# Kernel optimization log

Measured on AMD Instinct MI355X. Metric: run time of the kernel, lower is better.

The kernel has to match this reference:

```python
import jax, jax.numpy as jnp
import numpy as np

B, N, DIN, DOUT, K = 4, 2048, 512, 512, 3


def setup_inputs() -> dict:
    key = jax.random.key(0)
    ks = jax.random.split(key, 8)
    X = jax.random.normal(ks[0], (B, N, DIN), dtype=jnp.float32)
    A = jax.random.uniform(ks[1], (B, N, N), dtype=jnp.float32)
    # Linear_V: dimIn -> dimOut
    Wv = jax.random.normal(ks[2], (DIN, DOUT), dtype=jnp.float32) * 0.02
    bv = jax.random.normal(ks[3], (DOUT,), dtype=jnp.float32) * 0.02
    # alpha: Linear(2*dimOut -> 1) followed by LeakyReLU(0.2)
    aw = jax.random.normal(ks[4], (2 * DOUT, 1), dtype=jnp.float32) * 0.05
    ab = jax.random.normal(ks[5], (1,), dtype=jnp.float32) * 0.05
    # K parallel linears dimIn -> dimOut
    Wk = jax.random.normal(ks[6], (K, DIN, DOUT), dtype=jnp.float32) * 0.02
    bk = jax.random.normal(ks[7], (K, DOUT), dtype=jnp.float32) * 0.02
    return {"X": X, "A": A, "Wv": Wv, "bv": bv, "aw": aw, "ab": ab, "Wk": Wk, "bk": bk}


def reference(X, A, Wv, bv, aw, ab, Wk, bk):
    d = Wv.shape[1]
    Xw = X @ Wv + bv                      # (B, N, dOut)
    # att_input[b,i,j] = concat(Xw[b,j], Xw[b,i]); alpha is affine, so
    # alpha(att_input)[b,i,j] = aw1.Xw[b,j] + aw2.Xw[b,i] + ab  (GAT-style split)
    sj = Xw @ aw[:d, 0]                   # (B, N) contribution of column index j
    si = Xw @ aw[d:, 0]                   # (B, N) contribution of row index i
    e = jax.nn.leaky_relu(sj[:, None, :] + si[:, :, None] + ab[0], negative_slope=0.2)
    alpha_matrix = A * jnp.exp(e)         # (B, N, N)
    transition = alpha_matrix / (jnp.sum(alpha_matrix, axis=-1, keepdims=True) + 1e-12)
    H = jnp.zeros(X.shape[:-1] + (d,), dtype=X.dtype)
    Xk = X
    for k in range(Wk.shape[0]):          # K is a small static constant
        H = H + Xk @ Wk[k] + bk[k]
        Xk = jnp.einsum('bij,bjd->bid', transition, Xk)
    return jax.nn.relu(H)
```

## Files before the change

kernel.cpp:

```cpp
#include <hip/hip_runtime.h>

typedef float f32x4 __attribute__((ext_vector_type(4)));
typedef short s16x8 __attribute__((ext_vector_type(8)));
typedef unsigned short u16;
typedef unsigned char u8;
typedef u16 u16x4v __attribute__((ext_vector_type(4)));
typedef u16 u16x8v __attribute__((ext_vector_type(8)));

#define NB 4
#define NN 2048
#define DI 512
#define DOUTC 512
#define KP 3
#define KCAT 1536

__device__ __forceinline__ u16 f2b(float f) {
  unsigned u = __builtin_bit_cast(unsigned, f);
  unsigned r = u + 0x7fffu + ((u >> 16) & 1u);
  return (u16)(r >> 16);
}
__device__ __forceinline__ float b2f(u16 h) {
  unsigned u = (unsigned)h << 16;
  return __builtin_bit_cast(float, u);
}
__device__ __forceinline__ unsigned pk4_fp8(float a, float b, float c, float d) {
  int r = __builtin_amdgcn_cvt_pk_fp8_f32(a, b, 0, false);
  r = __builtin_amdgcn_cvt_pk_fp8_f32(c, d, r, true);
  return (unsigned)r;
}

__global__ void prep_all(const float* __restrict__ Wv, const float* __restrict__ aw,
                         const float* __restrict__ bk, const float* __restrict__ bv,
                         const float* __restrict__ ab,
                         float* u, float* v, float* bsum, float* cc) {
  if (blockIdx.x < 2) {
    int c = blockIdx.x * 256 + threadIdx.x;
    float a1 = 0.f, a2 = 0.f;
    const float* row = Wv + (size_t)c * DOUTC;
    for (int d = 0; d < DOUTC; ++d) {
      float w = row[d];
      a1 += w * aw[d];
      a2 += w * aw[DOUTC + d];
    }
    u[c] = a1; v[c] = a2;
    bsum[c] = bk[c] + bk[DOUTC + c] + bk[2 * DOUTC + c];
  } else if (threadIdx.x < 64) {
    int l = threadIdx.x;
    float s = 0.f;
    for (int d = l; d < DOUTC; d += 64) s += bv[d] * (aw[d] + aw[DOUTC + d]);
    for (int o = 32; o; o >>= 1) s += __shfl_down(s, o);
    if (l == 0) cc[0] = s + ab[0];
  }
}

__global__ void transWk_k(const float* __restrict__ in, u16* __restrict__ out) {
  __shared__ u16 tile[64][65];
  const float* inS = in + (size_t)blockIdx.z * DI * DOUTC;
  int r0 = blockIdx.y * 64, c0 = blockIdx.x * 64;
  int t = threadIdx.x;
#pragma unroll
  for (int p = 0; p < 4; ++p) {
    int g = t + p * 256;
    int r = g >> 4, c4 = (g & 15) << 2;
    f32x4 x = *(const f32x4*)(inS + (size_t)(r0 + r) * DOUTC + c0 + c4);
    tile[r][c4+0] = f2b(x[0]); tile[r][c4+1] = f2b(x[1]);
    tile[r][c4+2] = f2b(x[2]); tile[r][c4+3] = f2b(x[3]);
  }
  __syncthreads();
#pragma unroll
  for (int p = 0; p < 4; ++p) {
    int g = t + p * 256;
    int oc = g >> 4, o4 = (g & 15) << 2;
    u16x4v wv;
    wv[0] = tile[o4+0][oc]; wv[1] = tile[o4+1][oc];
    wv[2] = tile[o4+2][oc]; wv[3] = tile[o4+3][oc];
    *(u16x4v*)(out + (size_t)(c0 + oc) * KCAT + blockIdx.z * 512 + r0 + o4) = wv;
  }
}

__global__ void transX_k(const float* __restrict__ X, u8* __restrict__ XbT,
                         u16* __restrict__ X123,
                         const float* __restrict__ u, const float* __restrict__ v,
                         float* __restrict__ Pj, float* __restrict__ Pi) {
  __shared__ u16 tile[64][65];
  int z = blockIdx.z;
  const float* inS = X + (size_t)z * NN * DI;
  int r0 = blockIdx.y * 64, c0 = blockIdx.x * 64;
  int t = threadIdx.x, cl = t & 15;
  f32x4 u4 = *(const f32x4*)(u + c0 + cl * 4);
  f32x4 v4 = *(const f32x4*)(v + c0 + cl * 4);
#pragma unroll
  for (int p = 0; p < 4; ++p) {
    int g = t + p * 256;
    int r = g >> 4, c4 = cl << 2;
    f32x4 x = *(const f32x4*)(inS + (size_t)(r0 + r) * DI + c0 + c4);
    u16x4v bv4;
    bv4[0] = f2b(x[0]); bv4[1] = f2b(x[1]); bv4[2] = f2b(x[2]); bv4[3] = f2b(x[3]);
    tile[r][c4+0] = bv4[0]; tile[r][c4+1] = bv4[1];
    tile[r][c4+2] = bv4[2]; tile[r][c4+3] = bv4[3];
    *(u16x4v*)(X123 + (size_t)z * NN * KCAT + (size_t)(r0 + r) * KCAT + c0 + c4) = bv4;
    float s1 = x[0]*u4[0] + x[1]*u4[1] + x[2]*u4[2] + x[3]*u4[3];
    float s2 = x[0]*v4[0] + x[1]*v4[1] + x[2]*v4[2] + x[3]*v4[3];
#pragma unroll
    for (int m = 1; m < 16; m <<= 1) {
      s1 += __shfl_xor(s1, m);
      s2 += __shfl_xor(s2, m);
    }
    if (cl == 0) {
      int gr = z * NN + r0 + r;
      Pj[(size_t)blockIdx.x * (NB * NN) + gr] = s1;
      Pi[(size_t)blockIdx.x * (NB * NN) + gr] = s2;
    }
  }
  __syncthreads();
#pragma unroll
  for (int p = 0; p < 4; ++p) {
    int g = t + p * 256;
    int oc = g >> 4, o4 = (g & 15) << 2;
    unsigned w4 = pk4_fp8(b2f(tile[o4+0][oc]), b2f(tile[o4+1][oc]),
                          b2f(tile[o4+2][oc]), b2f(tile[o4+3][oc]));
    *(unsigned*)(XbT + (size_t)z * DI * NN + (size_t)(c0 + oc) * NN + r0 + o4) = w4;
  }
}

__global__ void sjsi_red(const float* __restrict__ Pj, const float* __restrict__ Pi,
                         float* __restrict__ sj, float* __restrict__ si) {
  int r = blockIdx.x * 256 + threadIdx.x;
  float s1 = 0.f, s2 = 0.f;
#pragma unroll
  for (int cb = 0; cb < 8; ++cb) {
    s1 += Pj[(size_t)cb * (NB * NN) + r];
    s2 += Pi[(size_t)cb * (NB * NN) + r];
  }
  sj[r] = s1; si[r] = s2;
}

__global__ void tmat_kernel(const float* __restrict__ Aa, const float* __restrict__ sj,
                            const float* __restrict__ si, const float* __restrict__ ccp,
                            u8* __restrict__ T, int rowbase) {
  int wid = threadIdx.x >> 6, lane = threadIdx.x & 63;
  int lr = blockIdx.x * 4 + wid;
  int gi = rowbase + lr;
  int b = gi >> 11;
  float siv = si[gi] + ccp[0];
  const f32x4* Arow = (const f32x4*)(Aa + (size_t)gi * NN);
  const f32x4* sjr = (const f32x4*)(sj + (size_t)b * NN);
  f32x4 al[8];
  float sum = 0.f;
#pragma unroll
  for (int t = 0; t < 8; ++t) {
    int f4 = lane + 64 * t;
    f32x4 a = Arow[f4];
    f32x4 s = sjr[f4];
#pragma unroll
    for (int j = 0; j < 4; ++j) {
      float e = s[j] + siv;
      e = e > 0.f ? e : 0.2f * e;
      al[t][j] = a[j] * __expf(e);
      sum += al[t][j];
    }
  }
#pragma unroll
  for (int o = 1; o < 64; o <<= 1) sum += __shfl_xor(sum, o);
  float rs = 256.0f / (sum + 1e-12f);
  u8* Trow = T + (size_t)lr * NN;
#pragma unroll
  for (int t = 0; t < 8; ++t) {
    int f4 = lane + 64 * t;
    unsigned w4 = pk4_fp8(al[t][0] * rs, al[t][1] * rs, al[t][2] * rs, al[t][3] * rs);
    *(unsigned*)(Trow + 4 * f4) = w4;
  }
}

__device__ __forceinline__ void gload16(const void* g, const void* l) {
  __builtin_amdgcn_global_load_lds((const __attribute__((address_space(1))) void*)g,
                                   (__attribute__((address_space(3))) void*)l, 16, 0, 0);
}

struct Gemm8P {
  const u8 *Ab;
  const u8 *Bb;
  u16* out;
  u8* outT;
  int ldA, ldB, ldO, ldOT;
  size_t batchA, batchB, batchOut, batchOutT;
  float osc, oscT;
};

template <int KT, bool OTR>
__launch_bounds__(256)
__global__ void gemm8_k(Gemm8P p) {
  __shared__ u8 As[3][128 * 128];
  __shared__ u8 Bs[3][64 * 128];
  int tid = threadIdx.x;
  int lane = tid & 63;
  int w = tid >> 6;
  int wr = w >> 1, wc = w & 1;
  int bm = blockIdx.x, bn = blockIdx.y, bz = blockIdx.z;
  int rof = lane & 15, ksel = lane >> 4, sw = lane & 7;
  int wub = (tid & 192) * 16;
  f32x4 acc[4][2] = {};
  const u8* Ag = p.Ab + (size_t)bz * p.batchA + (size_t)bm * 128 * p.ldA;
  const u8* Bg = p.Bb + (size_t)bz * p.batchB + (size_t)bn * 64 * p.ldB;

  auto stage = [&](int t, int buf) {
    int k0 = t * 128;
#pragma unroll
    for (int q = 0; q < 4; ++q) {
      int ch = q * 256 + tid;
      int row = ch >> 3;
      int c8 = (ch & 7) ^ (row & 7);
      gload16(Ag + (size_t)row * p.ldA + k0 + c8 * 16, &As[buf][0] + q * 4096 + wub);
    }
#pragma unroll
    for (int q = 0; q < 2; ++q) {
      int ch = q * 256 + tid;
      int row = ch >> 3;
      int c8 = (ch & 7) ^ (row & 7);
      gload16(Bg + (size_t)row * p.ldB + k0 + c8 * 16, &Bs[buf][0] + q * 4096 + wub);
    }
  };

  constexpr int TOT = KT;
  stage(0, 0);
  stage(1, 1);
  asm volatile("s_waitcnt vmcnt(6)" ::: "memory");
  __builtin_amdgcn_s_barrier();
  __builtin_amdgcn_sched_barrier(0);

  int bufc = 0;
  for (int t = 0; t < TOT; ++t) {
    int nb = t + 2;
    if (nb < TOT) stage(nb, bufc == 0 ? 2 : bufc - 1);
    const u8* Asb = &As[bufc][0];
    const u8* Bsb = &Bs[bufc][0];
#pragma unroll
    for (int kk = 0; kk < 4; ++kk) {
      int csw = ((2 * kk + (ksel >> 1)) ^ sw) * 16 + (ksel & 1) * 8;
      long af[4], bfr[2];
#pragma unroll
      for (int mf = 0; mf < 4; ++mf) {
        int r = wr * 64 + mf * 16 + rof;
        af[mf] = *(const long*)(Asb + (size_t)r * 128 + csw);
      }
#pragma unroll
      for (int nf = 0; nf < 2; ++nf) {
        int r = wc * 32 + nf * 16 + rof;
        bfr[nf] = *(const long*)(Bsb + (size_t)r * 128 + csw);
      }
#pragma unroll
      for (int mf = 0; mf < 4; ++mf)
#pragma unroll
        for (int nf = 0; nf < 2; ++nf)
          acc[mf][nf] = __builtin_amdgcn_mfma_f32_16x16x32_fp8_fp8(af[mf], bfr[nf], acc[mf][nf], 0, 0, 0);
    }
    if (nb < TOT) {
      asm volatile("s_waitcnt vmcnt(6)" ::: "memory");
    } else if (t + 1 < TOT) {
      asm volatile("s_waitcnt vmcnt(0)" ::: "memory");
    }
    if (t + 1 < TOT) {
      __builtin_amdgcn_s_barrier();
      __builtin_amdgcn_sched_barrier(0);
    }
    bufc = bufc + 1; if (bufc == 3) bufc = 0;
  }

  int rb = bm * 128 + wr * 64, cb = bn * 64 + wc * 32;
  int rsub = ksel << 2, csub = rof;
  u16* o = p.out + (size_t)bz * p.batchOut;
  u8* oT = OTR ? p.outT + (size_t)bz * p.batchOutT : nullptr;
#pragma unroll
  for (int mf = 0; mf < 4; ++mf)
#pragma unroll
    for (int nf = 0; nf < 2; ++nf) {
      int cidx = cb + nf * 16 + csub;
      f32x4 av = acc[mf][nf];
#pragma unroll
      for (int r = 0; r < 4; ++r)
        o[(size_t)(rb + mf * 16 + rsub + r) * p.ldO + cidx] = f2b(av[r] * p.osc);
      if constexpr (OTR) {
        unsigned w4 = pk4_fp8(av[0] * p.oscT, av[1] * p.oscT,
                              av[2] * p.oscT, av[3] * p.oscT);
        *(unsigned*)(oT + (size_t)cidx * p.ldOT + rb + mf * 16 + rsub) = w4;
      }
    }
}

struct GemmP {
  const u16 *A0, *A1, *A2;
  const u16 *B0, *B1, *B2;
  const float* bias;
  void* out;
  u16* outT;
  int ldA, ldB, ldO, ldOT;
  size_t batchA, batchB, batchOut, batchOutT;
};

template <int NSRC, int KT, bool OBF, bool OTR>
__launch_bounds__(256)
__global__ void gemm_k(GemmP p) {
  __shared__ u16 As[3][128 * 64];
  __shared__ u16 Bs[3][64 * 64];
  int tid = threadIdx.x;
  int lane = tid & 63;
  int w = tid >> 6;
  int wr = w >> 1, wc = w & 1;
  int bm = blockIdx.x, bn = blockIdx.y, bz = blockIdx.z;
  const u16* Alist[3] = {p.A0, p.A1, p.A2};
  const u16* Blist[3] = {p.B0, p.B1, p.B2};
  int rof = lane & 15, ksel = lane >> 4, sw = lane & 7;
  int wub = (tid & 192) * 8;
  f32x4 acc[4][2] = {};

  auto stage = [&](int t, int buf) {
    int s = t / KT;
    int k0 = (t - s * KT) * 64;
    const u16* Ag = Alist[s] + (size_t)bz * p.batchA + (size_t)bm * 128 * p.ldA;
    const u16* Bg = Blist[s] + (size_t)bz * p.batchB + (size_t)bn * 64 * p.ldB;
#pragma unroll
    for (int q = 0; q < 4; ++q) {
      int ch = q * 256 + tid;
      int row = ch >> 3;
      int c8 = (ch & 7) ^ (row & 7);
      gload16(Ag + (size_t)row * p.ldA + k0 + c8 * 8, &As[buf][0] + q * 2048 + wub);
    }
#pragma unroll
    for (int q = 0; q < 2; ++q) {
      int ch = q * 256 + tid;
      int row = ch >> 3;
      int c8 = (ch & 7) ^ (row & 7);
      gload16(Bg + (size_t)row * p.ldB + k0 + c8 * 8, &Bs[buf][0] + q * 2048 + wub);
    }
  };

  constexpr int TOT = NSRC * KT;
  stage(0, 0);
  stage(1, 1);
  asm volatile("s_waitcnt vmcnt(6)" ::: "memory");
  __builtin_amdgcn_s_barrier();
  __builtin_amdgcn_sched_barrier(0);

  int bufc = 0;
  for (int t = 0; t < TOT; ++t) {
    int nb = t + 2;
    if (nb < TOT) stage(nb, bufc == 0 ? 2 : bufc - 1);
    const u16* Asb = &As[bufc][0];
    const u16* Bsb = &Bs[bufc][0];
#pragma unroll
    for (int kk = 0; kk < 2; ++kk) {
      int csw = ((kk * 4 + ksel) ^ sw) * 8;
      s16x8 af[4], bfr[2];
#pragma unroll
      for (int mf = 0; mf < 4; ++mf) {
        int r = wr * 64 + mf * 16 + rof;
        af[mf] = *(const s16x8*)(Asb + r * 64 + csw);
      }
#pragma unroll
      for (int nf = 0; nf < 2; ++nf) {
        int r = wc * 32 + nf * 16 + rof;
        bfr[nf] = *(const s16x8*)(Bsb + r * 64 + csw);
      }
#pragma unroll
      for (int mf = 0; mf < 4; ++mf)
#pragma unroll
        for (int nf = 0; nf < 2; ++nf)
          acc[mf][nf] = __builtin_amdgcn_mfma_f32_16x16x32_bf16(af[mf], bfr[nf], acc[mf][nf], 0, 0, 0);
    }
    if (nb < TOT) {
      asm volatile("s_waitcnt vmcnt(6)" ::: "memory");
    } else if (t + 1 < TOT) {
      asm volatile("s_waitcnt vmcnt(0)" ::: "memory");
    }
    if (t + 1 < TOT) {
      __builtin_amdgcn_s_barrier();
      __builtin_amdgcn_sched_barrier(0);
    }
    bufc = bufc + 1; if (bufc == 3) bufc = 0;
  }

  int rb = bm * 128 + wr * 64, cb = bn * 64 + wc * 32;
  int rsub = ksel << 2, csub = rof;
  if constexpr (OBF) {
    u16* o = (u16*)p.out + (size_t)bz * p.batchOut;
    u16* oT = OTR ? p.outT + (size_t)bz * p.batchOutT : nullptr;
#pragma unroll
    for (int mf = 0; mf < 4; ++mf)
#pragma unroll
      for (int nf = 0; nf < 2; ++nf) {
        int cidx = cb + nf * 16 + csub;
        u16x4v tv;
#pragma unroll
        for (int r = 0; r < 4; ++r) {
          tv[r] = f2b(acc[mf][nf][r]);
          o[(size_t)(rb + mf * 16 + rsub + r) * p.ldO + cidx] = tv[r];
        }
        if constexpr (OTR) {
          *(u16x4v*)(oT + (size_t)cidx * p.ldOT + rb + mf * 16 + rsub) = tv;
        }
      }
  } else {
    float* o = (float*)p.out + (size_t)bz * p.batchOut;
#pragma unroll
    for (int nf = 0; nf < 2; ++nf) {
      int cidx = cb + nf * 16 + csub;
      float bv_ = p.bias[cidx];
#pragma unroll
      for (int mf = 0; mf < 4; ++mf)
#pragma unroll
        for (int r = 0; r < 4; ++r) {
          float val = acc[mf][nf][r] + bv_;
          o[(size_t)(rb + mf * 16 + rsub + r) * p.ldO + cidx] = val > 0.f ? val : 0.f;
        }
    }
  }
}

extern "C" void kernel_launch(void* const* d_in, const int* in_sizes, int n_in,
                              void* d_out, int out_size, void* d_ws, size_t ws_size,
                              hipStream_t stream) {
  const float* X  = (const float*)d_in[0];
  const float* A  = (const float*)d_in[1];
  const float* Wv = (const float*)d_in[2];
  const float* bv = (const float*)d_in[3];
  const float* aw = (const float*)d_in[4];
  const float* ab = (const float*)d_in[5];
  const float* Wk = (const float*)d_in[6];
  const float* bk = (const float*)d_in[7];
  float* out = (float*)d_out;

  char* ws = (char*)d_ws;
  size_t off = 0;
  auto alloc = [&](size_t bytes) -> void* {
    void* p = (void*)(ws + off);
    off = (off + bytes + 255) & ~(size_t)255;
    return p;
  };
  float* u    = (float*)alloc(DI * 4);
  float* v    = (float*)alloc(DI * 4);
  float* cc   = (float*)alloc(256);
  float* bsum = (float*)alloc(DOUTC * 4);
  float* sj   = (float*)alloc((size_t)NB * NN * 4);
  float* si   = (float*)alloc((size_t)NB * NN * 4);
  float* Pj   = (float*)alloc((size_t)8 * NB * NN * 4);
  float* Pi   = (float*)alloc((size_t)8 * NB * NN * 4);
  u16* BkT  = (u16*)alloc((size_t)DOUTC * KCAT * 2);
  u8*  XbT8 = (u8*)alloc((size_t)NB * DI * NN);
  u16* X123 = (u16*)alloc((size_t)NB * NN * KCAT * 2);
  u8*  X1bT8= (u8*)alloc((size_t)NB * DOUTC * NN);
  size_t fixedEnd = off;
  int G = 4;
  while (G > 1 && fixedEnd + (size_t)G * NN * NN > ws_size) G >>= 1;
  u8* Tb8 = (u8*)alloc((size_t)G * NN * NN);

  prep_all<<<3, 256, 0, stream>>>(Wv, aw, bk, bv, ab, u, v, bsum, cc);
  transWk_k<<<dim3(8, 8, 3), 256, 0, stream>>>(Wk, BkT);
  transX_k<<<dim3(8, 32, NB), 256, 0, stream>>>(X, XbT8, X123, u, v, Pj, Pi);
  sjsi_red<<<NB * NN / 256, 256, 0, stream>>>(Pj, Pi, sj, si);

  for (int g0 = 0; g0 < NB; g0 += G) {
    tmat_kernel<<<G * NN / 4, 256, 0, stream>>>(A, sj, si, cc, Tb8, g0 * NN);

    Gemm8P p1{};
    p1.Ab = Tb8;
    p1.Bb = XbT8 + (size_t)g0 * DI * NN;
    p1.out = X123 + (size_t)g0 * NN * KCAT + 512;
    p1.outT = X1bT8 + (size_t)g0 * DOUTC * NN;
    p1.ldA = NN; p1.ldB = NN; p1.ldO = KCAT; p1.ldOT = NN;
    p1.batchA = (size_t)NN * NN; p1.batchB = (size_t)DI * NN;
    p1.batchOut = (size_t)NN * KCAT; p1.batchOutT = (size_t)DOUTC * NN;
    p1.osc = 1.0f / 256.0f; p1.oscT = 16.0f / 256.0f;
    gemm8_k<16, true><<<dim3(16, 8, G), 256, 0, stream>>>(p1);

    Gemm8P p2 = p1;
    p2.Bb = X1bT8 + (size_t)g0 * DOUTC * NN;
    p2.out = X123 + (size_t)g0 * NN * KCAT + 1024;
    p2.outT = nullptr;
    p2.osc = 1.0f / 4096.0f;
    gemm8_k<16, false><<<dim3(16, 8, G), 256, 0, stream>>>(p2);
  }

  GemmP p3{};
  p3.A0 = p3.A1 = p3.A2 = X123;
  p3.B0 = p3.B1 = p3.B2 = BkT;
  p3.bias = bsum; p3.out = out; p3.outT = nullptr;
  p3.ldA = KCAT; p3.ldB = KCAT; p3.ldO = DOUTC; p3.ldOT = 0;
  p3.batchA = 0; p3.batchB = 0; p3.batchOut = 0; p3.batchOutT = 0;
  gemm_k<1, 24, false, false><<<dim3(64, 8, 1), 256, 0, stream>>>(p3);
}
```

Before: 113.4 us.

## Store propagated features and Wk in fp8 and use a mixed bf16/fp8 final GEMM

The X1 and X2 terms of the concatenated feature buffer, and the matching Wk blocks, are now stored as fp8 instead of bf16, and the X0 term stays bf16 in a byte-addressed row layout. The final GEMM becomes a mixed kernel that runs bf16 MFMA for the first half of K and fp8 MFMA for the rest, using separate accumulators that are rescaled and combined in the epilogue. This is meant to cut memory traffic and MFMA time in the final projection and in the epilogues of the propagation GEMMs. The cost is lower precision on the propagated terms and per-byte scattered stores in the gemm8 epilogue.

```diff
diff --git a/kernel.cpp b/kernel.cpp
--- a/kernel.cpp
+++ b/kernel.cpp
@@ -12,7 +12,7 @@
 #define DI 512
 #define DOUTC 512
 #define KP 3
-#define KCAT 1536
+#define ROWB 2048
 
 __device__ __forceinline__ u16 f2b(float f) {
   unsigned u = __builtin_bit_cast(unsigned, f);
@@ -53,9 +53,10 @@
   }
 }
 
-__global__ void transWk_k(const float* __restrict__ in, u16* __restrict__ out) {
+__global__ void transWk_k(const float* __restrict__ in, u8* __restrict__ out) {
   __shared__ u16 tile[64][65];
-  const float* inS = in + (size_t)blockIdx.z * DI * DOUTC;
+  int z = blockIdx.z;
+  const float* inS = in + (size_t)z * DI * DOUTC;
   int r0 = blockIdx.y * 64, c0 = blockIdx.x * 64;
   int t = threadIdx.x;
 #pragma unroll
@@ -71,15 +72,21 @@
   for (int p = 0; p < 4; ++p) {
     int g = t + p * 256;
     int oc = g >> 4, o4 = (g & 15) << 2;
-    u16x4v wv;
-    wv[0] = tile[o4+0][oc]; wv[1] = tile[o4+1][oc];
-    wv[2] = tile[o4+2][oc]; wv[3] = tile[o4+3][oc];
-    *(u16x4v*)(out + (size_t)(c0 + oc) * KCAT + blockIdx.z * 512 + r0 + o4) = wv;
+    if (z == 0) {
+      u16x4v wv;
+      wv[0] = tile[o4+0][oc]; wv[1] = tile[o4+1][oc];
+      wv[2] = tile[o4+2][oc]; wv[3] = tile[o4+3][oc];
+      *(u16x4v*)(out + (size_t)(c0 + oc) * ROWB + (size_t)(r0 + o4) * 2) = wv;
+    } else {
+      unsigned w4 = pk4_fp8(b2f(tile[o4+0][oc]) * 64.f, b2f(tile[o4+1][oc]) * 64.f,
+                            b2f(tile[o4+2][oc]) * 64.f, b2f(tile[o4+3][oc]) * 64.f);
+      *(unsigned*)(out + (size_t)(c0 + oc) * ROWB + 1024 + (z - 1) * 512 + r0 + o4) = w4;
+    }
   }
 }
 
 __global__ void transX_k(const float* __restrict__ X, u8* __restrict__ XbT,
-                         u16* __restrict__ X123,
+                         u8* __restrict__ X123B,
                          const float* __restrict__ u, const float* __restrict__ v,
                          float* __restrict__ Pj, float* __restrict__ Pi) {
   __shared__ u16 tile[64][65];
@@ -98,7 +105,8 @@
     bv4[0] = f2b(x[0]); bv4[1] = f2b(x[1]); bv4[2] = f2b(x[2]); bv4[3] = f2b(x[3]);
     tile[r][c4+0] = bv4[0]; tile[r][c4+1] = bv4[1];
     tile[r][c4+2] = bv4[2]; tile[r][c4+3] = bv4[3];
-    *(u16x4v*)(X123 + (size_t)z * NN * KCAT + (size_t)(r0 + r) * KCAT + c0 + c4) = bv4;
+    *(u16x4v*)(X123B + (size_t)z * NN * ROWB + (size_t)(r0 + r) * ROWB +
+               (size_t)(c0 + c4) * 2) = bv4;
     float s1 = x[0]*u4[0] + x[1]*u4[1] + x[2]*u4[2] + x[3]*u4[3];
     float s2 = x[0]*v4[0] + x[1]*v4[1] + x[2]*v4[2] + x[3]*v4[3];
 #pragma unroll
@@ -180,11 +188,11 @@
 struct Gemm8P {
   const u8 *Ab;
   const u8 *Bb;
-  u16* out;
+  u8* outR;
   u8* outT;
-  int ldA, ldB, ldO, ldOT;
-  size_t batchA, batchB, batchOut, batchOutT;
-  float osc, oscT;
+  int ldA, ldB, ldOB, ldOT;
+  size_t batchA, batchB, batchOutB, batchOutT;
+  float oscR;
 };
 
 template <int KT, bool OTR>
@@ -268,7 +276,7 @@
 
   int rb = bm * 128 + wr * 64, cb = bn * 64 + wc * 32;
   int rsub = ksel << 2, csub = rof;
-  u16* o = p.out + (size_t)bz * p.batchOut;
+  u8* o = p.outR + (size_t)bz * p.batchOutB;
   u8* oT = OTR ? p.outT + (size_t)bz * p.batchOutT : nullptr;
 #pragma unroll
   for (int mf = 0; mf < 4; ++mf)
@@ -276,65 +284,59 @@
     for (int nf = 0; nf < 2; ++nf) {
       int cidx = cb + nf * 16 + csub;
       f32x4 av = acc[mf][nf];
+      unsigned w4 = pk4_fp8(av[0] * p.oscR, av[1] * p.oscR,
+                            av[2] * p.oscR, av[3] * p.oscR);
 #pragma unroll
       for (int r = 0; r < 4; ++r)
-        o[(size_t)(rb + mf * 16 + rsub + r) * p.ldO + cidx] = f2b(av[r] * p.osc);
+        o[(size_t)(rb + mf * 16 + rsub + r) * p.ldOB + cidx] = (u8)(w4 >> (8 * r));
       if constexpr (OTR) {
-        unsigned w4 = pk4_fp8(av[0] * p.oscT, av[1] * p.oscT,
-                              av[2] * p.oscT, av[3] * p.oscT);
         *(unsigned*)(oT + (size_t)cidx * p.ldOT + rb + mf * 16 + rsub) = w4;
       }
     }
 }
 
-struct GemmP {
-  const u16 *A0, *A1, *A2;
-  const u16 *B0, *B1, *B2;
+struct GemmMixP {
+  const u8 *Ab;
+  const u8 *Bb;
   const float* bias;
-  void* out;
-  u16* outT;
-  int ldA, ldB, ldO, ldOT;
-  size_t batchA, batchB, batchOut, batchOutT;
+  float* out;
 };
 
-template <int NSRC, int KT, bool OBF, bool OTR>
 __launch_bounds__(256)
-__global__ void gemm_k(GemmP p) {
-  __shared__ u16 As[3][128 * 64];
-  __shared__ u16 Bs[3][64 * 64];
+__global__ void gemm_mix_k(GemmMixP p) {
+  __shared__ u8 As[3][128 * 128];
+  __shared__ u8 Bs[3][64 * 128];
   int tid = threadIdx.x;
   int lane = tid & 63;
   int w = tid >> 6;
   int wr = w >> 1, wc = w & 1;
-  int bm = blockIdx.x, bn = blockIdx.y, bz = blockIdx.z;
-  const u16* Alist[3] = {p.A0, p.A1, p.A2};
-  const u16* Blist[3] = {p.B0, p.B1, p.B2};
+  int bm = blockIdx.x, bn = blockIdx.y;
   int rof = lane & 15, ksel = lane >> 4, sw = lane & 7;
-  int wub = (tid & 192) * 8;
-  f32x4 acc[4][2] = {};
+  int wub = (tid & 192) * 16;
+  f32x4 accB[4][2] = {};
+  f32x4 acc8[4][2] = {};
+  const u8* Ag = p.Ab + (size_t)bm * 128 * ROWB;
+  const u8* Bg = p.Bb + (size_t)bn * 64 * ROWB;
 
   auto stage = [&](int t, int buf) {
-    int s = t / KT;
-    int k0 = (t - s * KT) * 64;
-    const u16* Ag = Alist[s] + (size_t)bz * p.batchA + (size_t)bm * 128 * p.ldA;
-    const u16* Bg = Blist[s] + (size_t)bz * p.batchB + (size_t)bn * 64 * p.ldB;
+    int k0 = t * 128;
 #pragma unroll
     for (int q = 0; q < 4; ++q) {
       int ch = q * 256 + tid;
       int row = ch >> 3;
       int c8 = (ch & 7) ^ (row & 7);
-      gload16(Ag + (size_t)row * p.ldA + k0 + c8 * 8, &As[buf][0] + q * 2048 + wub);
+      gload16(Ag + (size_t)row * ROWB + k0 + c8 * 16, &As[buf][0] + q * 4096 + wub);
     }
 #pragma unroll
     for (int q = 0; q < 2; ++q) {
       int ch = q * 256 + tid;
       int row = ch >> 3;
       int c8 = (ch & 7) ^ (row & 7);
-      gload16(Bg + (size_t)row * p.ldB + k0 + c8 * 8, &Bs[buf][0] + q * 2048 + wub);
+      gload16(Bg + (size_t)row * ROWB + k0 + c8 * 16, &Bs[buf][0] + q * 4096 + wub);
     }
   };
 
-  constexpr int TOT = NSRC * KT;
+  constexpr int TOT = 16;
   stage(0, 0);
   stage(1, 1);
   asm volatile("s_waitcnt vmcnt(6)" ::: "memory");
@@ -345,27 +347,50 @@
   for (int t = 0; t < TOT; ++t) {
     int nb = t + 2;
     if (nb < TOT) stage(nb, bufc == 0 ? 2 : bufc - 1);
-    const u16* Asb = &As[bufc][0];
-    const u16* Bsb = &Bs[bufc][0];
-#pragma unroll
-    for (int kk = 0; kk < 2; ++kk) {
-      int csw = ((kk * 4 + ksel) ^ sw) * 8;
-      s16x8 af[4], bfr[2];
-#pragma unroll
-      for (int mf = 0; mf < 4; ++mf) {
-        int r = wr * 64 + mf * 16 + rof;
-        af[mf] = *(const s16x8*)(Asb + r * 64 + csw);
-      }
-#pragma unroll
-      for (int nf = 0; nf < 2; ++nf) {
-        int r = wc * 32 + nf * 16 + rof;
-        bfr[nf] = *(const s16x8*)(Bsb + r * 64 + csw);
-      }
-#pragma unroll
-      for (int mf = 0; mf < 4; ++mf)
-#pragma unroll
-        for (int nf = 0; nf < 2; ++nf)
-          acc[mf][nf] = __builtin_amdgcn_mfma_f32_16x16x32_bf16(af[mf], bfr[nf], acc[mf][nf], 0, 0, 0);
+    const u8* Asb = &As[bufc][0];
+    const u8* Bsb = &Bs[bufc][0];
+    if (t < 8) {
+#pragma unroll
+      for (int kk = 0; kk < 2; ++kk) {
+        int csw = ((kk * 4 + ksel) ^ sw) * 16;
+        s16x8 af[4], bfr[2];
+#pragma unroll
+        for (int mf = 0; mf < 4; ++mf) {
+          int r = wr * 64 + mf * 16 + rof;
+          af[mf] = *(const s16x8*)(Asb + (size_t)r * 128 + csw);
+        }
+#pragma unroll
+        for (int nf = 0; nf < 2; ++nf) {
+          int r = wc * 32 + nf * 16 + rof;
+          bfr[nf] = *(const s16x8*)(Bsb + (size_t)r * 128 + csw);
+        }
+#pragma unroll
+        for (int mf = 0; mf < 4; ++mf)
+#pragma unroll
+          for (int nf = 0; nf < 2; ++nf)
+            accB[mf][nf] = __builtin_amdgcn_mfma_f32_16x16x32_bf16(af[mf], bfr[nf], accB[mf][nf], 0, 0, 0);
+      }
+    } else {
+#pragma unroll
+      for (int kk = 0; kk < 4; ++kk) {
+        int csw = ((2 * kk + (ksel >> 1)) ^ sw) * 16 + (ksel & 1) * 8;
+        long af[4], bfr[2];
+#pragma unroll
+        for (int mf = 0; mf < 4; ++mf) {
+          int r = wr * 64 + mf * 16 + rof;
+          af[mf] = *(const long*)(Asb + (size_t)r * 128 + csw);
+        }
+#pragma unroll
+        for (int nf = 0; nf < 2; ++nf) {
+          int r = wc * 32 + nf * 16 + rof;
+          bfr[nf] = *(const long*)(Bsb + (size_t)r * 128 + csw);
+        }
+#pragma unroll
+        for (int mf = 0; mf < 4; ++mf)
+#pragma unroll
+          for (int nf = 0; nf < 2; ++nf)
+            acc8[mf][nf] = __builtin_amdgcn_mfma_f32_16x16x32_fp8_fp8(af[mf], bfr[nf], acc8[mf][nf], 0, 0, 0);
+      }
     }
     if (nb < TOT) {
       asm volatile("s_waitcnt vmcnt(6)" ::: "memory");
@@ -381,38 +406,18 @@
 
   int rb = bm * 128 + wr * 64, cb = bn * 64 + wc * 32;
   int rsub = ksel << 2, csub = rof;
-  if constexpr (OBF) {
-    u16* o = (u16*)p.out + (size_t)bz * p.batchOut;
-    u16* oT = OTR ? p.outT + (size_t)bz * p.batchOutT : nullptr;
+  const float inv = 1.0f / 1024.0f;
+#pragma unroll
+  for (int nf = 0; nf < 2; ++nf) {
+    int cidx = cb + nf * 16 + csub;
+    float bv_ = p.bias[cidx];
 #pragma unroll
     for (int mf = 0; mf < 4; ++mf)
 #pragma unroll
-      for (int nf = 0; nf < 2; ++nf) {
-        int cidx = cb + nf * 16 + csub;
-        u16x4v tv;
-#pragma unroll
-        for (int r = 0; r < 4; ++r) {
-          tv[r] = f2b(acc[mf][nf][r]);
-          o[(size_t)(rb + mf * 16 + rsub + r) * p.ldO + cidx] = tv[r];
-        }
-        if constexpr (OTR) {
-          *(u16x4v*)(oT + (size_t)cidx * p.ldOT + rb + mf * 16 + rsub) = tv;
-        }
-      }
-  } else {
-    float* o = (float*)p.out + (size_t)bz * p.batchOut;
-#pragma unroll
-    for (int nf = 0; nf < 2; ++nf) {
-      int cidx = cb + nf * 16 + csub;
-      float bv_ = p.bias[cidx];
-#pragma unroll
-      for (int mf = 0; mf < 4; ++mf)
-#pragma unroll
-        for (int r = 0; r < 4; ++r) {
-          float val = acc[mf][nf][r] + bv_;
-          o[(size_t)(rb + mf * 16 + rsub + r) * p.ldO + cidx] = val > 0.f ? val : 0.f;
-        }
-    }
+      for (int r = 0; r < 4; ++r) {
+        float val = accB[mf][nf][r] + acc8[mf][nf][r] * inv + bv_;
+        p.out[(size_t)(rb + mf * 16 + rsub + r) * DOUTC + cidx] = val > 0.f ? val : 0.f;
+      }
   }
 }
 
@@ -444,18 +449,18 @@
   float* si   = (float*)alloc((size_t)NB * NN * 4);
   float* Pj   = (float*)alloc((size_t)8 * NB * NN * 4);
   float* Pi   = (float*)alloc((size_t)8 * NB * NN * 4);
-  u16* BkT  = (u16*)alloc((size_t)DOUTC * KCAT * 2);
-  u8*  XbT8 = (u8*)alloc((size_t)NB * DI * NN);
-  u16* X123 = (u16*)alloc((size_t)NB * NN * KCAT * 2);
-  u8*  X1bT8= (u8*)alloc((size_t)NB * DOUTC * NN);
+  u8* BkTB  = (u8*)alloc((size_t)DOUTC * ROWB);
+  u8* XbT8  = (u8*)alloc((size_t)NB * DI * NN);
+  u8* X123B = (u8*)alloc((size_t)NB * NN * ROWB);
+  u8* X1bT8 = (u8*)alloc((size_t)NB * DOUTC * NN);
   size_t fixedEnd = off;
   int G = 4;
   while (G > 1 && fixedEnd + (size_t)G * NN * NN > ws_size) G >>= 1;
   u8* Tb8 = (u8*)alloc((size_t)G * NN * NN);
 
   prep_all<<<3, 256, 0, stream>>>(Wv, aw, bk, bv, ab, u, v, bsum, cc);
-  transWk_k<<<dim3(8, 8, 3), 256, 0, stream>>>(Wk, BkT);
-  transX_k<<<dim3(8, 32, NB), 256, 0, stream>>>(X, XbT8, X123, u, v, Pj, Pi);
+  transWk_k<<<dim3(8, 8, 3), 256, 0, stream>>>(Wk, BkTB);
+  transX_k<<<dim3(8, 32, NB), 256, 0, stream>>>(X, XbT8, X123B, u, v, Pj, Pi);
   sjsi_red<<<NB * NN / 256, 256, 0, stream>>>(Pj, Pi, sj, si);
 
   for (int g0 = 0; g0 < NB; g0 += G) {
@@ -464,27 +469,23 @@
     Gemm8P p1{};
     p1.Ab = Tb8;
     p1.Bb = XbT8 + (size_t)g0 * DI * NN;
-    p1.out = X123 + (size_t)g0 * NN * KCAT + 512;
+    p1.outR = X123B + (size_t)g0 * NN * ROWB + 1024;
     p1.outT = X1bT8 + (size_t)g0 * DOUTC * NN;
-    p1.ldA = NN; p1.ldB = NN; p1.ldO = KCAT; p1.ldOT = NN;
+    p1.ldA = NN; p1.ldB = NN; p1.ldOB = ROWB; p1.ldOT = NN;
     p1.batchA = (size_t)NN * NN; p1.batchB = (size_t)DI * NN;
-    p1.batchOut = (size_t)NN * KCAT; p1.batchOutT = (size_t)DOUTC * NN;
-    p1.osc = 1.0f / 256.0f; p1.oscT = 16.0f / 256.0f;
+    p1.batchOutB = (size_t)NN * ROWB; p1.batchOutT = (size_t)DOUTC * NN;
+    p1.oscR = 16.0f / 256.0f;
     gemm8_k<16, true><<<dim3(16, 8, G), 256, 0, stream>>>(p1);
 
     Gemm8P p2 = p1;
     p2.Bb = X1bT8 + (size_t)g0 * DOUTC * NN;
-    p2.out = X123 + (size_t)g0 * NN * KCAT + 1024;
+    p2.outR = X123B + (size_t)g0 * NN * ROWB + 1536;
     p2.outT = nullptr;
-    p2.osc = 1.0f / 4096.0f;
+    p2.oscR = 16.0f / 4096.0f;
     gemm8_k<16, false><<<dim3(16, 8, G), 256, 0, stream>>>(p2);
   }
 
-  GemmP p3{};
-  p3.A0 = p3.A1 = p3.A2 = X123;
-  p3.B0 = p3.B1 = p3.B2 = BkT;
-  p3.bias = bsum; p3.out = out; p3.outT = nullptr;
-  p3.ldA = KCAT; p3.ldB = KCAT; p3.ldO = DOUTC; p3.ldOT = 0;
-  p3.batchA = 0; p3.batchB = 0; p3.batchOut = 0; p3.batchOutT = 0;
-  gemm_k<1, 24, false, false><<<dim3(64, 8, 1), 256, 0, stream>>>(p3);
-}
+  GemmMixP p3{};
+  p3.Ab = X123B; p3.Bb = BkTB; p3.bias = bsum; p3.out = out;
+  gemm_mix_k<<<dim3(64, 8, 1), 256, 0, stream>>>(p3);
+}
```

After: 109.4 us. 3.6% less time.
